# Kernel tuning notes

Hardware: AMD Instinct MI355X
Metric: run time of the kernel (lower is better)

Reference implementation:

```python
import jax, jax.numpy as jnp
import numpy as np

D_MODEL = 1024
NUM_HEADS = 16
MAX_LEN = 2048
HEAD_DIM = D_MODEL // NUM_HEADS
BATCH = 4
SEQ = 1024


def setup_inputs() -> dict:
    key = jax.random.key(0)
    ks = jax.random.split(key, 5)
    return {
        "query": jax.random.normal(ks[0], (BATCH, SEQ, D_MODEL), dtype=jnp.float32),
        "key": jax.random.normal(ks[1], (BATCH, SEQ, D_MODEL), dtype=jnp.float32),
        "value": jax.random.normal(ks[2], (BATCH, SEQ, D_MODEL), dtype=jnp.float32),
        "rel_k": jax.random.normal(ks[3], (MAX_LEN, HEAD_DIM), dtype=jnp.float32),
        "rel_v": jax.random.normal(ks[4], (MAX_LEN, HEAD_DIM), dtype=jnp.float32),
    }


def reference(query, key, value, rel_k, rel_v):
    B, S, D = query.shape
    H, hd = NUM_HEADS, D // NUM_HEADS
    # (B, H, S, hd)
    q = query.reshape(B, S, H, hd).transpose(0, 2, 1, 3)
    k = key.reshape(B, S, H, hd).transpose(0, 2, 1, 3)
    v = value.reshape(B, S, H, hd).transpose(0, 2, 1, 3)
    scale = 1.0 / np.sqrt(hd).astype(np.float32)
    # content scores + relative-position key bias (q . rel_k)
    scores = jnp.einsum("bhqd,bhkd->bhqk", q, k) * scale
    scores = scores + jnp.einsum("bhqd,kd->bhqk", q, rel_k[:S])
    attn = jax.nn.softmax(scores, axis=-1)  # (B, H, S, S)
    out = jnp.einsum("bhqk,bhkd->bhqd", attn, v)
    out = out + jnp.einsum("bhqk,kd->bhqd", attn, rel_v[:S])
    return out.transpose(0, 2, 1, 3).reshape(B, S, D)
```

## Files before the change

kernel.cpp:

```cpp
#include <hip/hip_runtime.h>

#define SQ 1024
#define DM 1024
#define HD 64
#define NBH 64
#define LOG2E 1.44269504f

typedef __attribute__((ext_vector_type(8))) _Float16 v8h;
typedef __attribute__((ext_vector_type(4))) float v4f;
typedef __attribute__((ext_vector_type(4))) unsigned int v4u;

typedef __attribute__((address_space(3))) void as3_void;
typedef __attribute__((address_space(1))) const void as1_cvoid;

__device__ __forceinline__ v4f mfma_f16(v8h a, v8h b, v4f c) {
  return __builtin_amdgcn_mfma_f32_16x16x32_f16(a, b, c, 0, 0, 0);
}

__device__ __forceinline__ void gload16(const _Float16* g, v8h* l) {
  __builtin_amdgcn_global_load_lds((as1_cvoid*)g, (as3_void*)l, 16, 0, 0);
}

__device__ __forceinline__ float m3(float a, float b, float c) {
  return fmaxf(fmaxf(a, b), c);
}

__global__ __launch_bounds__(256) void prep_kernel(
    const float* __restrict__ q, const float* __restrict__ k, const float* __restrict__ v,
    const float* __restrict__ relk, const float* __restrict__ relv,
    _Float16* __restrict__ Qh, _Float16* __restrict__ Kh,
    _Float16* __restrict__ Vth)
{
  __shared__ float vt[64][65];
  int blk = blockIdx.x;
  int st = blk & 15;
  int bh = blk >> 4;
  int b = bh >> 4, h = bh & 15;
  int s0 = st * 64;
  int t = (int)threadIdx.x;
  int d = t & 63, sl4 = t >> 6;
  const float scale = 0.125f;

  #pragma unroll
  for (int i = 0; i < 16; ++i) {
    int sl = sl4 + i * 4;
    int s = s0 + sl;
    size_t gidx = ((size_t)(b * SQ + s)) * DM + h * HD + d;
    float qv = q[gidx];
    float kv = (k[gidx] * scale + relk[s * HD + d]) * LOG2E;
    float vv = v[gidx] + relv[s * HD + d];
    size_t widx = ((size_t)(bh * SQ + s)) * HD + d;
    Qh[widx] = (_Float16)qv;
    Kh[widx] = (_Float16)kv;
    vt[sl][d] = vv;
  }
  __syncthreads();
  int sl = t & 63, d4 = t >> 6;
  #pragma unroll
  for (int i = 0; i < 16; ++i) {
    int dd = d4 + i * 4;
    Vth[((size_t)(bh * HD + dd)) * SQ + s0 + sl] = (_Float16)vt[sl][dd];
  }
}

__global__ __launch_bounds__(256) void attn_kernel(
    const _Float16* __restrict__ Qh, const _Float16* __restrict__ Kh,
    const _Float16* __restrict__ Vth, float* __restrict__ out)
{
  __shared__ v8h KlG[2 * 512];
  __shared__ v8h VlG[2 * 512];

  int tid = (int)threadIdx.x;
  int lane = tid & 63, w = tid >> 6;
  int g = lane >> 4, r15 = lane & 15;
  int bid = (int)blockIdx.x;
  int wk = (bid & 7) * 128 + (bid >> 3);
  int bh = wk >> 4, qt = wk & 15;
  int b = bh >> 4, h = bh & 15;
  int q0 = qt * 64 + w * 16;

  const _Float16* qb = Qh + ((size_t)(bh * SQ + q0 + r15)) * HD;
  v8h aq0 = *(const v8h*)(qb + g * 8);
  v8h aq1 = *(const v8h*)(qb + 32 + g * 8);

  const _Float16* kb = Kh + (size_t)bh * SQ * HD;
  const _Float16* vb = Vth + (size_t)bh * HD * SQ;

  size_t kOff[2], vOff[2];
  int ldsG[2];
  #pragma unroll
  for (int j = 0; j < 2; ++j) {
    int G = w * 128 + j * 64 + lane;
    int row = G >> 3, gr = G & 7;
    int fs = (row & 3) | (((row >> 3) & 1) << 2);
    int src = gr ^ fs;
    kOff[j] = (size_t)row * HD + src * 8;
    vOff[j] = (size_t)row * SQ + src * 8;
    ldsG[j] = w * 128 + j * 64;
  }

  v4f o[4];
  #pragma unroll
  for (int c = 0; c < 4; ++c) o[c] = (v4f){0.f, 0.f, 0.f, 0.f};
  float m = -3.0e38f, l = 0.f;

  int krow[4];
  #pragma unroll
  for (int c = 0; c < 4; ++c)
    krow[c] = ((c >> 1) << 5) + ((r15 >> 2) << 3) + ((c & 1) << 2) + (r15 & 3);
  int fk = (r15 & 3) | (((r15 >> 2) & 1) << 2);
  int fv = (r15 & 3) | (((r15 >> 3) & 1) << 2);

  const int NT = SQ / 64;

  #pragma unroll
  for (int j = 0; j < 2; ++j) {
    gload16(kb + kOff[j], &KlG[ldsG[j]]);
    gload16(vb + vOff[j], &VlG[ldsG[j]]);
  }
  __syncthreads();

  for (int t0 = 0; t0 < NT; ++t0) {
    int cur = t0 & 1;
    if (t0 < NT - 1) {
      size_t kT = (size_t)(t0 + 1) * 64 * HD;
      size_t vT = (size_t)(t0 + 1) * 64;
      #pragma unroll
      for (int j = 0; j < 2; ++j) {
        gload16(kb + kT + kOff[j], &KlG[(cur ^ 1) * 512 + ldsG[j]]);
        gload16(vb + vT + vOff[j], &VlG[(cur ^ 1) * 512 + ldsG[j]]);
      }
    }

    v4f s[4];
    #pragma unroll
    for (int c = 0; c < 4; ++c) {
      v8h kf0 = KlG[cur * 512 + krow[c] * 8 + (g ^ fk)];
      v8h kf1 = KlG[cur * 512 + krow[c] * 8 + ((4 | g) ^ fk)];
      v4f z = (v4f){0.f, 0.f, 0.f, 0.f};
      z = mfma_f16(kf0, aq0, z);
      z = mfma_f16(kf1, aq1, z);
      s[c] = z;
    }

    float pa = m3(s[0][0], s[0][1], s[0][2]);
    float pb = m3(s[0][3], s[1][0], s[1][1]);
    float pc = m3(s[1][2], s[1][3], s[2][0]);
    float pd = m3(s[2][1], s[2][2], s[2][3]);
    float pe = m3(s[3][0], s[3][1], s[3][2]);
    float pm = m3(fmaxf(pa, pb), fmaxf(pc, pd), fmaxf(pe, s[3][3]));
    if (!__all(pm - m <= 8.f)) {
      float pmr = fmaxf(pm, __shfl_xor(pm, 16));
      pmr = fmaxf(pmr, __shfl_xor(pmr, 32));
      float mnew = fmaxf(m, pmr);
      float sc = __builtin_amdgcn_exp2f(m - mnew);
      m = mnew;
      l *= sc;
      #pragma unroll
      for (int c = 0; c < 4; ++c) o[c] *= sc;
    }
    float p[16];
    #pragma unroll
    for (int c = 0; c < 4; ++c)
      #pragma unroll
      for (int r = 0; r < 4; ++r) {
        float pv = __builtin_amdgcn_exp2f(s[c][r] - m);
        s[c][r] = pv;
        p[c * 4 + r] = pv;
      }
    float s0 = (p[0] + p[1]) + (p[2] + p[3]);
    float s1 = (p[4] + p[5]) + (p[6] + p[7]);
    float s2 = (p[8] + p[9]) + (p[10] + p[11]);
    float s3 = (p[12] + p[13]) + (p[14] + p[15]);
    l += (s0 + s1) + (s2 + s3);

    v4u w0, w1;
    w0[0] = __builtin_bit_cast(unsigned int, __builtin_amdgcn_cvt_pkrtz(s[0][0], s[0][1]));
    w0[1] = __builtin_bit_cast(unsigned int, __builtin_amdgcn_cvt_pkrtz(s[0][2], s[0][3]));
    w0[2] = __builtin_bit_cast(unsigned int, __builtin_amdgcn_cvt_pkrtz(s[1][0], s[1][1]));
    w0[3] = __builtin_bit_cast(unsigned int, __builtin_amdgcn_cvt_pkrtz(s[1][2], s[1][3]));
    w1[0] = __builtin_bit_cast(unsigned int, __builtin_amdgcn_cvt_pkrtz(s[2][0], s[2][1]));
    w1[1] = __builtin_bit_cast(unsigned int, __builtin_amdgcn_cvt_pkrtz(s[2][2], s[2][3]));
    w1[2] = __builtin_bit_cast(unsigned int, __builtin_amdgcn_cvt_pkrtz(s[3][0], s[3][1]));
    w1[3] = __builtin_bit_cast(unsigned int, __builtin_amdgcn_cvt_pkrtz(s[3][2], s[3][3]));
    v8h pb0 = __builtin_bit_cast(v8h, w0);
    v8h pb1 = __builtin_bit_cast(v8h, w1);

    #pragma unroll
    for (int c = 0; c < 4; ++c) {
      int rv = 16 * c + r15;
      v8h vf0 = VlG[cur * 512 + rv * 8 + (g ^ fv)];
      v8h vf1 = VlG[cur * 512 + rv * 8 + ((4 | g) ^ fv)];
      o[c] = mfma_f16(vf0, pb0, o[c]);
      o[c] = mfma_f16(vf1, pb1, o[c]);
    }

    __syncthreads();
  }

  float lr = l;
  lr += __shfl_xor(lr, 16);
  lr += __shfl_xor(lr, 32);
  float inv = 1.f / lr;
  int qrow = q0 + r15;
  #pragma unroll
  for (int c = 0; c < 4; ++c) {
    v4f res = o[c] * inv;
    *(v4f*)(&out[((size_t)(b * SQ + qrow)) * DM + h * HD + 16 * c + 4 * g]) = res;
  }
}

extern "C" void kernel_launch(void* const* d_in, const int* in_sizes, int n_in,
                              void* d_out, int out_size, void* d_ws, size_t ws_size,
                              hipStream_t stream) {
  const float* q = (const float*)d_in[0];
  const float* k = (const float*)d_in[1];
  const float* v = (const float*)d_in[2];
  const float* relk = (const float*)d_in[3];
  const float* relv = (const float*)d_in[4];

  _Float16* Qh = (_Float16*)d_ws;
  _Float16* Kh = Qh + (size_t)NBH * SQ * HD;
  _Float16* Vth = Kh + (size_t)NBH * SQ * HD;

  prep_kernel<<<dim3(NBH * (SQ / 64)), dim3(256), 0, stream>>>(q, k, v, relk, relv, Qh, Kh, Vth);
  attn_kernel<<<dim3(1024), dim3(256), 0, stream>>>(Qh, Kh, Vth, (float*)d_out);
}
```

Measured before the change: 50.76 us.

## Switch attention to 32x32x16 MFMA with 2 waves of 32 query rows

Replaces the 16x16x32 MFMA tiling (4 waves x 16 query rows) with 32x32x16 MFMA tiles (2 waves x 32 query rows per block), changing the register layout of scores and outputs. The V transpose in the prep kernel permutes sequence positions so P fragments line up with the new accumulator layout, and the LDS swizzle is simplified. The larger MFMA shape is meant to raise matrix throughput per instruction and reuse each K/V fragment load across more rows. The cost is fewer waves per block, doubled per-thread global-to-LDS loads and higher register pressure.

After: 52.40 us. +3.2%, slower.

```diff
diff --git a/kernel.cpp b/kernel.cpp
--- a/kernel.cpp
+++ b/kernel.cpp
@@ -8,21 +8,18 @@
 
 typedef __attribute__((ext_vector_type(8))) _Float16 v8h;
 typedef __attribute__((ext_vector_type(4))) float v4f;
+typedef __attribute__((ext_vector_type(16))) float v16f;
 typedef __attribute__((ext_vector_type(4))) unsigned int v4u;
 
 typedef __attribute__((address_space(3))) void as3_void;
 typedef __attribute__((address_space(1))) const void as1_cvoid;
 
-__device__ __forceinline__ v4f mfma_f16(v8h a, v8h b, v4f c) {
-  return __builtin_amdgcn_mfma_f32_16x16x32_f16(a, b, c, 0, 0, 0);
+__device__ __forceinline__ v16f mfma32(v8h a, v8h b, v16f c) {
+  return __builtin_amdgcn_mfma_f32_32x32x16_f16(a, b, c, 0, 0, 0);
 }
 
 __device__ __forceinline__ void gload16(const _Float16* g, v8h* l) {
   __builtin_amdgcn_global_load_lds((as1_cvoid*)g, (as3_void*)l, 16, 0, 0);
-}
-
-__device__ __forceinline__ float m3(float a, float b, float c) {
-  return fmaxf(fmaxf(a, b), c);
 }
 
 __global__ __launch_bounds__(256) void prep_kernel(
@@ -56,14 +53,15 @@
   }
   __syncthreads();
   int sl = t & 63, d4 = t >> 6;
+  int swp = (sl & 51) | ((sl & 4) << 1) | ((sl & 8) >> 1);
   #pragma unroll
   for (int i = 0; i < 16; ++i) {
     int dd = d4 + i * 4;
-    Vth[((size_t)(bh * HD + dd)) * SQ + s0 + sl] = (_Float16)vt[sl][dd];
-  }
-}
-
-__global__ __launch_bounds__(256) void attn_kernel(
+    Vth[((size_t)(bh * HD + dd)) * SQ + s0 + swp] = (_Float16)vt[sl][dd];
+  }
+}
+
+__global__ __launch_bounds__(128) void attn_kernel(
     const _Float16* __restrict__ Qh, const _Float16* __restrict__ Kh,
     const _Float16* __restrict__ Vth, float* __restrict__ out)
 {
@@ -72,51 +70,45 @@
 
   int tid = (int)threadIdx.x;
   int lane = tid & 63, w = tid >> 6;
-  int g = lane >> 4, r15 = lane & 15;
+  int q31 = lane & 31, half = lane >> 5;
   int bid = (int)blockIdx.x;
   int wk = (bid & 7) * 128 + (bid >> 3);
   int bh = wk >> 4, qt = wk & 15;
   int b = bh >> 4, h = bh & 15;
-  int q0 = qt * 64 + w * 16;
-
-  const _Float16* qb = Qh + ((size_t)(bh * SQ + q0 + r15)) * HD;
-  v8h aq0 = *(const v8h*)(qb + g * 8);
-  v8h aq1 = *(const v8h*)(qb + 32 + g * 8);
+  int qrow = qt * 64 + w * 32 + q31;
+
+  const _Float16* qb = Qh + ((size_t)(bh * SQ + qrow)) * HD + 8 * half;
+  v8h aq[4];
+  #pragma unroll
+  for (int cc = 0; cc < 4; ++cc) aq[cc] = *(const v8h*)(qb + 16 * cc);
 
   const _Float16* kb = Kh + (size_t)bh * SQ * HD;
   const _Float16* vb = Vth + (size_t)bh * HD * SQ;
 
-  size_t kOff[2], vOff[2];
-  int ldsG[2];
-  #pragma unroll
-  for (int j = 0; j < 2; ++j) {
-    int G = w * 128 + j * 64 + lane;
+  size_t kOff[4], vOff[4];
+  int ldsG[4];
+  #pragma unroll
+  for (int i = 0; i < 4; ++i) {
+    int G = w * 64 + i * 128 + lane;
     int row = G >> 3, gr = G & 7;
-    int fs = (row & 3) | (((row >> 3) & 1) << 2);
-    int src = gr ^ fs;
-    kOff[j] = (size_t)row * HD + src * 8;
-    vOff[j] = (size_t)row * SQ + src * 8;
-    ldsG[j] = w * 128 + j * 64;
-  }
-
-  v4f o[4];
-  #pragma unroll
-  for (int c = 0; c < 4; ++c) o[c] = (v4f){0.f, 0.f, 0.f, 0.f};
+    int src = gr ^ (row & 7);
+    kOff[i] = (size_t)row * HD + src * 8;
+    vOff[i] = (size_t)row * SQ + src * 8;
+    ldsG[i] = w * 64 + i * 128;
+  }
+
+  v16f o0 = {0.f,0.f,0.f,0.f,0.f,0.f,0.f,0.f,0.f,0.f,0.f,0.f,0.f,0.f,0.f,0.f};
+  v16f o1 = o0;
   float m = -3.0e38f, l = 0.f;
 
-  int krow[4];
-  #pragma unroll
-  for (int c = 0; c < 4; ++c)
-    krow[c] = ((c >> 1) << 5) + ((r15 >> 2) << 3) + ((c & 1) << 2) + (r15 & 3);
-  int fk = (r15 & 3) | (((r15 >> 2) & 1) << 2);
-  int fv = (r15 & 3) | (((r15 >> 3) & 1) << 2);
+  int rx = q31 & 7;
 
   const int NT = SQ / 64;
 
   #pragma unroll
-  for (int j = 0; j < 2; ++j) {
-    gload16(kb + kOff[j], &KlG[ldsG[j]]);
-    gload16(vb + vOff[j], &VlG[ldsG[j]]);
+  for (int i = 0; i < 4; ++i) {
+    gload16(kb + kOff[i], &KlG[ldsG[i]]);
+    gload16(vb + vOff[i], &VlG[ldsG[i]]);
   }
   __syncthreads();
 
@@ -126,87 +118,90 @@
       size_t kT = (size_t)(t0 + 1) * 64 * HD;
       size_t vT = (size_t)(t0 + 1) * 64;
       #pragma unroll
-      for (int j = 0; j < 2; ++j) {
-        gload16(kb + kT + kOff[j], &KlG[(cur ^ 1) * 512 + ldsG[j]]);
-        gload16(vb + vT + vOff[j], &VlG[(cur ^ 1) * 512 + ldsG[j]]);
+      for (int i = 0; i < 4; ++i) {
+        gload16(kb + kT + kOff[i], &KlG[(cur ^ 1) * 512 + ldsG[i]]);
+        gload16(vb + vT + vOff[i], &VlG[(cur ^ 1) * 512 + ldsG[i]]);
       }
     }
 
-    v4f s[4];
-    #pragma unroll
-    for (int c = 0; c < 4; ++c) {
-      v8h kf0 = KlG[cur * 512 + krow[c] * 8 + (g ^ fk)];
-      v8h kf1 = KlG[cur * 512 + krow[c] * 8 + ((4 | g) ^ fk)];
-      v4f z = (v4f){0.f, 0.f, 0.f, 0.f};
-      z = mfma_f16(kf0, aq0, z);
-      z = mfma_f16(kf1, aq1, z);
-      s[c] = z;
-    }
-
-    float pa = m3(s[0][0], s[0][1], s[0][2]);
-    float pb = m3(s[0][3], s[1][0], s[1][1]);
-    float pc = m3(s[1][2], s[1][3], s[2][0]);
-    float pd = m3(s[2][1], s[2][2], s[2][3]);
-    float pe = m3(s[3][0], s[3][1], s[3][2]);
-    float pm = m3(fmaxf(pa, pb), fmaxf(pc, pd), fmaxf(pe, s[3][3]));
+    v16f s0v = o0 * 0.f;
+    v16f s1v = s0v;
+    #pragma unroll
+    for (int cc = 0; cc < 4; ++cc) {
+      v8h kf0 = KlG[cur * 512 + (q31) * 8 + ((2 * cc + half) ^ rx)];
+      v8h kf1 = KlG[cur * 512 + (32 + q31) * 8 + ((2 * cc + half) ^ rx)];
+      s0v = mfma32(kf0, aq[cc], s0v);
+      s1v = mfma32(kf1, aq[cc], s1v);
+    }
+
+    float sc32[32];
+    #pragma unroll
+    for (int r = 0; r < 16; ++r) { sc32[r] = s0v[r]; sc32[16 + r] = s1v[r]; }
+    float mx[16];
+    #pragma unroll
+    for (int r = 0; r < 16; ++r) mx[r] = fmaxf(sc32[2 * r], sc32[2 * r + 1]);
+    #pragma unroll
+    for (int r = 0; r < 8; ++r) mx[r] = fmaxf(mx[r], mx[r + 8]);
+    #pragma unroll
+    for (int r = 0; r < 4; ++r) mx[r] = fmaxf(mx[r], mx[r + 4]);
+    float pm = fmaxf(fmaxf(mx[0], mx[1]), fmaxf(mx[2], mx[3]));
     if (!__all(pm - m <= 8.f)) {
-      float pmr = fmaxf(pm, __shfl_xor(pm, 16));
-      pmr = fmaxf(pmr, __shfl_xor(pmr, 32));
+      float pmr = fmaxf(pm, __shfl_xor(pm, 32));
       float mnew = fmaxf(m, pmr);
       float sc = __builtin_amdgcn_exp2f(m - mnew);
       m = mnew;
       l *= sc;
+      o0 *= sc;
+      o1 *= sc;
+    }
+    #pragma unroll
+    for (int r = 0; r < 32; ++r)
+      sc32[r] = __builtin_amdgcn_exp2f(sc32[r] - m);
+    float ad[16];
+    #pragma unroll
+    for (int r = 0; r < 16; ++r) ad[r] = sc32[2 * r] + sc32[2 * r + 1];
+    #pragma unroll
+    for (int r = 0; r < 8; ++r) ad[r] += ad[r + 8];
+    #pragma unroll
+    for (int r = 0; r < 4; ++r) ad[r] += ad[r + 4];
+    l += (ad[0] + ad[1]) + (ad[2] + ad[3]);
+
+    v8h pb[4];
+    #pragma unroll
+    for (int c = 0; c < 4; ++c) {
+      v4u wds;
       #pragma unroll
-      for (int c = 0; c < 4; ++c) o[c] *= sc;
-    }
-    float p[16];
-    #pragma unroll
-    for (int c = 0; c < 4; ++c)
-      #pragma unroll
-      for (int r = 0; r < 4; ++r) {
-        float pv = __builtin_amdgcn_exp2f(s[c][r] - m);
-        s[c][r] = pv;
-        p[c * 4 + r] = pv;
-      }
-    float s0 = (p[0] + p[1]) + (p[2] + p[3]);
-    float s1 = (p[4] + p[5]) + (p[6] + p[7]);
-    float s2 = (p[8] + p[9]) + (p[10] + p[11]);
-    float s3 = (p[12] + p[13]) + (p[14] + p[15]);
-    l += (s0 + s1) + (s2 + s3);
-
-    v4u w0, w1;
-    w0[0] = __builtin_bit_cast(unsigned int, __builtin_amdgcn_cvt_pkrtz(s[0][0], s[0][1]));
-    w0[1] = __builtin_bit_cast(unsigned int, __builtin_amdgcn_cvt_pkrtz(s[0][2], s[0][3]));
-    w0[2] = __builtin_bit_cast(unsigned int, __builtin_amdgcn_cvt_pkrtz(s[1][0], s[1][1]));
-    w0[3] = __builtin_bit_cast(unsigned int, __builtin_amdgcn_cvt_pkrtz(s[1][2], s[1][3]));
-    w1[0] = __builtin_bit_cast(unsigned int, __builtin_amdgcn_cvt_pkrtz(s[2][0], s[2][1]));
-    w1[1] = __builtin_bit_cast(unsigned int, __builtin_amdgcn_cvt_pkrtz(s[2][2], s[2][3]));
-    w1[2] = __builtin_bit_cast(unsigned int, __builtin_amdgcn_cvt_pkrtz(s[3][0], s[3][1]));
-    w1[3] = __builtin_bit_cast(unsigned int, __builtin_amdgcn_cvt_pkrtz(s[3][2], s[3][3]));
-    v8h pb0 = __builtin_bit_cast(v8h, w0);
-    v8h pb1 = __builtin_bit_cast(v8h, w1);
+      for (int r = 0; r < 4; ++r)
+        wds[r] = __builtin_bit_cast(unsigned int,
+                   __builtin_amdgcn_cvt_pkrtz(sc32[c * 8 + 2 * r], sc32[c * 8 + 2 * r + 1]));
+      pb[c] = __builtin_bit_cast(v8h, wds);
+    }
 
     #pragma unroll
     for (int c = 0; c < 4; ++c) {
-      int rv = 16 * c + r15;
-      v8h vf0 = VlG[cur * 512 + rv * 8 + (g ^ fv)];
-      v8h vf1 = VlG[cur * 512 + rv * 8 + ((4 | g) ^ fv)];
-      o[c] = mfma_f16(vf0, pb0, o[c]);
-      o[c] = mfma_f16(vf1, pb1, o[c]);
+      v8h vf0 = VlG[cur * 512 + (q31) * 8 + ((2 * c + half) ^ rx)];
+      v8h vf1 = VlG[cur * 512 + (32 + q31) * 8 + ((2 * c + half) ^ rx)];
+      o0 = mfma32(vf0, pb[c], o0);
+      o1 = mfma32(vf1, pb[c], o1);
     }
 
     __syncthreads();
   }
 
-  float lr = l;
-  lr += __shfl_xor(lr, 16);
-  lr += __shfl_xor(lr, 32);
+  float lr = l + __shfl_xor(l, 32);
   float inv = 1.f / lr;
-  int qrow = q0 + r15;
-  #pragma unroll
-  for (int c = 0; c < 4; ++c) {
-    v4f res = o[c] * inv;
-    *(v4f*)(&out[((size_t)(b * SQ + qrow)) * DM + h * HD + 16 * c + 4 * g]) = res;
+  float* ob = out + ((size_t)(b * SQ + qrow)) * DM + h * HD;
+  #pragma unroll
+  for (int rq = 0; rq < 4; ++rq) {
+    v4f r0, r1;
+    #pragma unroll
+    for (int j = 0; j < 4; ++j) {
+      r0[j] = o0[4 * rq + j] * inv;
+      r1[j] = o1[4 * rq + j] * inv;
+    }
+    int d0 = 8 * rq + 4 * half;
+    *(v4f*)(ob + d0) = r0;
+    *(v4f*)(ob + 32 + d0) = r1;
   }
 }
 
@@ -224,5 +219,5 @@
   _Float16* Vth = Kh + (size_t)NBH * SQ * HD;
 
   prep_kernel<<<dim3(NBH * (SQ / 64)), dim3(256), 0, stream>>>(q, k, v, relk, relv, Qh, Kh, Vth);
-  attn_kernel<<<dim3(1024), dim3(256), 0, stream>>>(Qh, Kh, Vth, (float*)d_out);
-}
+  attn_kernel<<<dim3(1024), dim3(128), 0, stream>>>(Qh, Kh, Vth, (float*)d_out);
+}
```
